# Kernel tuning notes

Measured on AMD Instinct MI355X. Metric: run time of the kernel, lower is better.

Reference implementation:

```python
import jax, jax.numpy as jnp
import numpy as np

N = 100000   # nodes
E = 1000000  # edges
G = 64       # graphs in batch
DIN, DH, DOUT = 128, 128, 64
BN_EPS = 1e-5


def setup_inputs() -> dict:
    key = jax.random.key(0)
    ks = jax.random.split(key, 20)
    inp = {}
    inp['x'] = jax.random.normal(ks[0], (N, DIN), dtype=jnp.float32)
    inp['edge_index'] = jax.random.randint(ks[1], (2, E), 0, N, dtype=jnp.int64)
    inp['batch'] = jnp.sort(jax.random.randint(ks[2], (N,), 0, G, dtype=jnp.int64))
    # GCN conv weights (stored [in, out]) + biases
    s = lambda k, i, o: jax.random.normal(k, (i, o), dtype=jnp.float32) / np.sqrt(i)
    inp['W1'] = s(ks[3], DIN, DH);  inp['b1'] = jnp.zeros((DH,), jnp.float32)
    inp['W2'] = s(ks[4], DH, DH);   inp['b2'] = jnp.zeros((DH,), jnp.float32)
    inp['W3'] = s(ks[5], DH, DOUT); inp['b3'] = jnp.zeros((DOUT,), jnp.float32)
    # BatchNorm params/buffers (eval mode)
    inp['g1'] = jnp.ones((DH,), jnp.float32);  inp['beta1'] = jnp.zeros((DH,), jnp.float32)
    inp['g2'] = jnp.ones((DH,), jnp.float32);  inp['beta2'] = jnp.zeros((DH,), jnp.float32)
    inp['mean1'] = jnp.zeros((DH,), jnp.float32); inp['var1'] = jnp.ones((DH,), jnp.float32)
    inp['mean2'] = jnp.zeros((DH,), jnp.float32); inp['var2'] = jnp.ones((DH,), jnp.float32)
    # GlobalAttention gate_nn: Linear(DOUT,DH) ReLU Linear(DH,1)
    inp['Wg1'] = s(ks[6], DOUT, DH); inp['bg1'] = jnp.zeros((DH,), jnp.float32)
    inp['Wg2'] = s(ks[7], DH, 1);    inp['bg2'] = jnp.zeros((1,), jnp.float32)
    # head MLP: Linear(DOUT,DH) ReLU Linear(DH,DOUT)
    inp['Wm1'] = s(ks[8], DOUT, DH); inp['bm1'] = jnp.zeros((DH,), jnp.float32)
    inp['Wm2'] = s(ks[9], DH, DOUT); inp['bm2'] = jnp.zeros((DOUT,), jnp.float32)
    return inp


def _gcn_conv(x, W, b, src, dst):
    # PyG GCNConv: add self-loops, sym-normalize, linear, scatter-sum, bias
    h = x @ W                                            # [N, out]
    deg = jnp.ones((N,), h.dtype).at[dst].add(1.0)       # in-degree + self-loop
    dinv = jax.lax.rsqrt(deg)
    norm = dinv[src] * dinv[dst]                         # [E]
    msg = h[src] * norm[:, None]                         # gather + scale
    out = jax.ops.segment_sum(msg, dst, num_segments=N)  # scatter
    out = out + h * (dinv * dinv)[:, None]               # self-loop term
    return out + b


def _bn(x, g, beta, mean, var):
    return (x - mean) * jax.lax.rsqrt(var + BN_EPS) * g + beta


def reference(x, edge_index, batch, W1, b1, W2, b2, W3, b3,
              g1, beta1, g2, beta2, mean1, var1, mean2, var2,
              Wg1, bg1, Wg2, bg2, Wm1, bm1, Wm2, bm2):
    src, dst = edge_index[0], edge_index[1]
    h = jax.nn.relu(_bn(_gcn_conv(x, W1, b1, src, dst), g1, beta1, mean1, var1))
    h = jax.nn.relu(_bn(_gcn_conv(h, W2, b2, src, dst), g2, beta2, mean2, var2))
    h = _gcn_conv(h, W3, b3, src, dst)                   # [N, DOUT]
    # GlobalAttention pooling: per-graph softmax of gate scores
    gate = jax.nn.relu(h @ Wg1 + bg1) @ Wg2 + bg2        # [N, 1]
    gate = gate[:, 0]
    m = jax.ops.segment_max(gate, batch, num_segments=G)
    e = jnp.exp(gate - m[batch])
    s = jax.ops.segment_sum(e, batch, num_segments=G)
    a = e / s[batch]                                     # [N]
    pooled = jax.ops.segment_sum(h * a[:, None], batch, num_segments=G)  # [G, DOUT]
    # MLP head (dropout off in eval)
    return jax.nn.relu(pooled @ Wm1 + bm1) @ Wm2 + bm2   # [G, DOUT]
```

## Files before the change

kernel.cpp:

```cpp
#include <hip/hip_runtime.h>
#include <hip/hip_bf16.h>
#include <hip/hip_fp16.h>
#include <math.h>

#define NN 100000
#define EE 1000000
#define GG 64
#define BN_EPS 1e-5f
#define CPB 16
#define EB 4096
#define NBLK ((EE + EB - 1) / EB)
#define NBUCK ((NN + 511) / 512)

typedef __attribute__((ext_vector_type(8))) short bf16x8;
typedef __attribute__((ext_vector_type(4))) float f32x4;

__device__ inline short f2bf(float f) {
  unsigned u = __float_as_uint(f);
  u = u + 0x7fff + ((u >> 16) & 1);
  return (short)(u >> 16);
}
__device__ inline float bf2f(short h) {
  return __uint_as_float(((unsigned)(unsigned short)h) << 16);
}

__device__ inline unsigned fenc(float f) {
  int b = __float_as_int(f);
  return (b < 0) ? ~(unsigned)b : ((unsigned)b | 0x80000000u);
}
__device__ inline float fdec(unsigned u) {
  int b = (u & 0x80000000u) ? (int)(u & 0x7fffffffu) : (int)~u;
  return __int_as_float(b);
}

__device__ inline void acc2(float& a0, float& a1, unsigned u) {
  asm("v_fma_mix_f32 %0, %2, 1.0, %0 op_sel:[0,0,0] op_sel_hi:[1,0,0]\n\t"
      "v_fma_mix_f32 %1, %2, 1.0, %1 op_sel:[1,0,0] op_sel_hi:[1,0,0]"
      : "+v"(a0), "+v"(a1)
      : "v"(u));
}
__device__ inline void acc8(float* a, uint4 u) {
  acc2(a[0], a[1], u.x);
  acc2(a[2], a[3], u.y);
  acc2(a[4], a[5], u.z);
  acc2(a[6], a[7], u.w);
}
__device__ inline uint4 zsel(uint4 u, int ok) {
  uint4 r;
  r.x = ok ? u.x : 0u;
  r.y = ok ? u.y : 0u;
  r.z = ok ? u.z : 0u;
  r.w = ok ? u.w : 0u;
  return r;
}

__global__ __launch_bounds__(256) void k_bhist(const int* __restrict__ dst,
                                               int* __restrict__ bhist, int E) {
  __shared__ int h[256];
  int t = threadIdx.x;
  h[t] = 0;
  __syncthreads();
  int base = blockIdx.x * EB;
#pragma unroll
  for (int j = 0; j < EB / 256; ++j) {
    int i = base + j * 256 + t;
    if (i < E) atomicAdd(&h[dst[i] >> 9], 1);
  }
  __syncthreads();
  bhist[blockIdx.x * 256 + t] = h[t];
}

__global__ __launch_bounds__(256) void k_bscan1(int* __restrict__ bhist,
                                                int* __restrict__ btot) {
  __shared__ int s[256];
  int bin = blockIdx.x, t = threadIdx.x;
  int v = (t < NBLK) ? bhist[t * 256 + bin] : 0;
  s[t] = v;
  __syncthreads();
  for (int o = 1; o < 256; o <<= 1) {
    int u = (t >= o) ? s[t - o] : 0;
    __syncthreads();
    s[t] += u;
    __syncthreads();
  }
  if (t < NBLK) bhist[t * 256 + bin] = s[t] - v;
  if (t == 255) btot[bin] = s[255];
}

__global__ __launch_bounds__(256) void k_bscan2(const int* __restrict__ btot,
                                                int* __restrict__ bstart) {
  __shared__ int s[256];
  int t = threadIdx.x;
  int v = btot[t];
  s[t] = v;
  __syncthreads();
  for (int o = 1; o < 256; o <<= 1) {
    int u = (t >= o) ? s[t - o] : 0;
    __syncthreads();
    s[t] += u;
    __syncthreads();
  }
  bstart[t] = s[t] - v;
}

__global__ __launch_bounds__(256) void k_bscat(const int* __restrict__ src,
                                               const int* __restrict__ dst,
                                               const int* __restrict__ bhist,
                                               const int* __restrict__ bstart,
                                               int2* __restrict__ pairs, int E) {
  __shared__ int h[256];
  __shared__ int base[256];
  int t = threadIdx.x;
  h[t] = 0;
  __syncthreads();
  int b0 = blockIdx.x * EB;
  int ds[EB / 256], rk[EB / 256];
#pragma unroll
  for (int j = 0; j < EB / 256; ++j) {
    int i = b0 + j * 256 + t;
    if (i < E) {
      int d = dst[i];
      ds[j] = d;
      rk[j] = atomicAdd(&h[d >> 9], 1);
    } else
      ds[j] = -1;
  }
  __syncthreads();
  base[t] = bstart[t] + bhist[blockIdx.x * 256 + t];
  __syncthreads();
#pragma unroll
  for (int j = 0; j < EB / 256; ++j) {
    int i = b0 + j * 256 + t;
    if (ds[j] >= 0) {
      int pos = base[ds[j] >> 9] + rk[j];
      pairs[pos] = make_int2(src[i], ds[j]);
    }
  }
}

__global__ __launch_bounds__(256) void k_bfill(const int2* __restrict__ pairs,
                                               const int* __restrict__ bstart,
                                               int* __restrict__ rowstart,
                                               int* __restrict__ eidx,
                                               float* __restrict__ dinv, int N,
                                               int E) {
  __shared__ int h[512];
  __shared__ int ex[512];
  __shared__ int ps[256];
  const int b = blockIdx.x;
  const int n0 = b << 9;
  const int e0 = bstart[b], e1 = bstart[b + 1];
  const int t = threadIdx.x;
  h[t] = 0;
  h[t + 256] = 0;
  __syncthreads();
  for (int i = e0 + t; i < e1; i += 256) atomicAdd(&h[pairs[i].y - n0], 1);
  __syncthreads();
  int v0 = h[2 * t], v1 = h[2 * t + 1];
  int sp = v0 + v1;
  ps[t] = sp;
  __syncthreads();
  for (int o = 1; o < 256; o <<= 1) {
    int u = (t >= o) ? ps[t - o] : 0;
    __syncthreads();
    ps[t] += u;
    __syncthreads();
  }
  int ex0 = ps[t] - sp;
  ex[2 * t] = ex0;
  ex[2 * t + 1] = ex0 + v0;
  __syncthreads();
  for (int i = t; i < 512; i += 256) {
    int node = n0 + i;
    if (node < N) {
      rowstart[node] = e0 + ex[i];
      dinv[node] = rsqrtf(1.0f + (float)h[i]);
    }
  }
  if (b == 0 && t == 0) rowstart[N] = E;
  __syncthreads();
  for (int i = e0 + t; i < e1; i += 256) {
    int2 p = pairs[i];
    int r = atomicAdd(&ex[p.y - n0], 1);
    eidx[e0 + r] = p.x;
  }
}

__global__ __launch_bounds__(256) void k_wsplit(const float* __restrict__ W1,
                                                const float* __restrict__ W2,
                                                const float* __restrict__ W3,
                                                const float* __restrict__ Wg1,
                                                short* __restrict__ wt) {
  int i = blockIdx.x * 256 + threadIdx.x;
  const float* W;
  short *hi, *lo;
  int K, M, idx;
  if (i < 16384) {
    W = W1; hi = wt; lo = wt + 16384; K = 128; M = 128; idx = i;
  } else if (i < 32768) {
    W = W2; hi = wt + 32768; lo = wt + 49152; K = 128; M = 128; idx = i - 16384;
  } else if (i < 40960) {
    W = W3; hi = wt + 65536; lo = wt + 73728; K = 128; M = 64; idx = i - 32768;
  } else {
    W = Wg1; hi = wt + 81920; lo = wt + 90112; K = 64; M = 128; idx = i - 40960;
  }
  int k = idx / M, n = idx % M;
  float w = W[idx];
  short h = f2bf(w);
  hi[n * K + k] = h;
  lo[n * K + k] = f2bf(w - bf2f(h));
}

__global__ __launch_bounds__(256) void k_bnprep(
    const float* __restrict__ g1, const float* __restrict__ b1,
    const float* __restrict__ m1, const float* __restrict__ v1,
    const float* __restrict__ g2, const float* __restrict__ b2,
    const float* __restrict__ m2, const float* __restrict__ v2,
    float* __restrict__ s1, float* __restrict__ h1, float* __restrict__ s2,
    float* __restrict__ h2) {
  int i = threadIdx.x;
  if (i < 128) {
    float s = g1[i] * rsqrtf(v1[i] + BN_EPS);
    s1[i] = s;
    h1[i] = b1[i] - m1[i] * s;
  } else {
    int j = i - 128;
    float s = g2[j] * rsqrtf(v2[j] + BN_EPS);
    s2[j] = s;
    h2[j] = b2[j] - m2[j] * s;
  }
}

template <int K, int M, int CTB, int AIN, int DINV, int GATE, int OUTH>
__device__ __forceinline__ void mgemm_body(
    short* lds, const float* __restrict__ Xf, const short* __restrict__ Xhi,
    const short* __restrict__ Xlo, const short* __restrict__ Wthi,
    const short* __restrict__ Wtlo, const float* __restrict__ dinv,
    const float* __restrict__ gbias, const float* __restrict__ Wg2v,
    const float* __restrict__ bg2v, void* __restrict__ Y,
    float* __restrict__ gate, int nrows) {
  constexpr int NC = K / 32;
  constexpr int KP = K + 8;
  constexpr int R = 2;
  const int lane = threadIdx.x & 63;
  const int wave = threadIdx.x >> 6;
  const int m16 = lane & 15;
  const int quad = lane >> 4;
  const int rowbase = blockIdx.x * 128 + wave * 32;
  const int cbase = blockIdx.y * CTB * 16;

  bf16x8 ahi[R][NC], alo[R][NC];
#pragma unroll
  for (int t = 0; t < R; ++t) {
    const int arow = rowbase + t * 16 + m16;
    const bool rok = arow < nrows;
#pragma unroll
    for (int c = 0; c < NC; ++c) {
      const int k0 = c * 32 + quad * 8;
      if constexpr (AIN) {
        if (rok) {
          ahi[t][c] = *(const bf16x8*)(Xhi + (size_t)arow * K + k0);
          alo[t][c] = *(const bf16x8*)(Xlo + (size_t)arow * K + k0);
        } else {
          ahi[t][c] = bf16x8{0, 0, 0, 0, 0, 0, 0, 0};
          alo[t][c] = bf16x8{0, 0, 0, 0, 0, 0, 0, 0};
        }
      } else {
        float4 v0 = make_float4(0.f, 0.f, 0.f, 0.f), v1 = v0;
        if (rok) {
          v0 = *(const float4*)(Xf + (size_t)arow * K + k0);
          v1 = *(const float4*)(Xf + (size_t)arow * K + k0 + 4);
        }
        float vv[8] = {v0.x, v0.y, v0.z, v0.w, v1.x, v1.y, v1.z, v1.w};
#pragma unroll
        for (int j = 0; j < 8; ++j) {
          short h = f2bf(vv[j]);
          ahi[t][c][j] = h;
          alo[t][c][j] = f2bf(vv[j] - bf2f(h));
        }
      }
    }
  }

  {
    constexpr int ELEMS = CTB * 16 * K;
#pragma unroll
    for (int i = threadIdx.x * 8; i < ELEMS; i += 256 * 8) {
      const int r = i / K, c = i % K;
      *(bf16x8*)(&lds[r * KP + c]) =
          *(const bf16x8*)(Wthi + (size_t)(cbase + r) * K + c);
      *(bf16x8*)(&lds[CTB * 16 * KP + r * KP + c]) =
          *(const bf16x8*)(Wtlo + (size_t)(cbase + r) * K + c);
    }
  }

  float dv[R][4];
  if constexpr (DINV && !GATE) {
#pragma unroll
    for (int t = 0; t < R; ++t)
#pragma unroll
      for (int r = 0; r < 4; ++r) {
        int row = rowbase + t * 16 + quad * 4 + r;
        dv[t][r] = (row < nrows) ? dinv[row] : 0.f;
      }
  }

  float gp[R][4];
  if constexpr (GATE) {
#pragma unroll
    for (int t = 0; t < R; ++t)
#pragma unroll
      for (int r = 0; r < 4; ++r) gp[t][r] = 0.f;
  }

  __syncthreads();

  f32x4 accs[CTB][R];
#pragma unroll
  for (int ct = 0; ct < CTB; ++ct) {
    bf16x8 bhi[NC], blo[NC];
    const int wrow = (ct * 16 + m16) * KP + quad * 8;
#pragma unroll
    for (int c = 0; c < NC; ++c) {
      bhi[c] = *(const bf16x8*)(&lds[wrow + c * 32]);
      blo[c] = *(const bf16x8*)(&lds[CTB * 16 * KP + wrow + c * 32]);
    }
#pragma unroll
    for (int t = 0; t < R; ++t) {
      f32x4 acc = {0.f, 0.f, 0.f, 0.f};
#pragma unroll
      for (int c = 0; c < NC; ++c) {
        acc = __builtin_amdgcn_mfma_f32_16x16x32_bf16(ahi[t][c], bhi[c], acc, 0, 0, 0);
        acc = __builtin_amdgcn_mfma_f32_16x16x32_bf16(ahi[t][c], blo[c], acc, 0, 0, 0);
        acc = __builtin_amdgcn_mfma_f32_16x16x32_bf16(alo[t][c], bhi[c], acc, 0, 0, 0);
      }
      if constexpr (GATE) {
        const int col = cbase + ct * 16 + m16;
        const float gb = gbias[col], wg = Wg2v[col];
#pragma unroll
        for (int r = 0; r < 4; ++r) gp[t][r] += fmaxf(acc[r] + gb, 0.f) * wg;
      } else {
        accs[ct][t] = acc;
      }
    }
  }

  if constexpr (GATE) {
#pragma unroll
    for (int o = 1; o < 16; o <<= 1) {
#pragma unroll
      for (int t = 0; t < R; ++t)
#pragma unroll
        for (int r = 0; r < 4; ++r) gp[t][r] += __shfl_xor(gp[t][r], o, 64);
    }
    if (m16 == 0) {
      const float b2 = bg2v[0];
#pragma unroll
      for (int t = 0; t < R; ++t)
#pragma unroll
        for (int r = 0; r < 4; ++r) {
          const int row = rowbase + t * 16 + quad * 4 + r;
          if (row < nrows) gate[row] = gp[t][r] + b2;
        }
    }
  } else {
    constexpr int COLS = CTB * 16;
    constexpr int SP = COLS + 8;
    __syncthreads();
#pragma unroll
    for (int ct = 0; ct < CTB; ++ct)
#pragma unroll
      for (int t = 0; t < R; ++t)
#pragma unroll
        for (int r = 0; r < 4; ++r) {
          const int row_l = wave * 32 + t * 16 + quad * 4 + r;
          float v = accs[ct][t][r];
          if constexpr (DINV) v *= dv[t][r];
          __half hv = __float2half(v);
          lds[row_l * SP + ct * 16 + m16] = *(short*)&hv;
        }
    __syncthreads();
    constexpr int TOT = 128 * COLS;
#pragma unroll
    for (int p = 0; p < TOT / (256 * 8); ++p) {
      const int idx8 = (p * 256 + threadIdx.x) * 8;
      const int row_l = idx8 / COLS;
      const int col0 = idx8 % COLS;
      const int grow = blockIdx.x * 128 + row_l;
      if (grow < nrows) {
        bf16x8 v = *(const bf16x8*)(&lds[row_l * SP + col0]);
        *(bf16x8*)((__half*)Y + (size_t)grow * M + cbase + col0) = v;
      }
    }
  }
}

#define MGEMM_ARGS                                                            \
  const float *Xf, const short *Xhi, const short *Xlo, const short *Wthi,     \
      const short *Wtlo, const float *dinv, const float *gbias,               \
      const float *Wg2v, const float *bg2v, void *Y, float *gate, int nrows

#define DEF_MGEMM(NAME, K, M, CTB, AIN, DINV, GATE, OUTH)                     \
  __global__ __launch_bounds__(256, 3) void NAME(MGEMM_ARGS) {                \
    __shared__ short lds[2 * CTB * 16 * (K + 8)];                             \
    mgemm_body<K, M, CTB, AIN, DINV, GATE, OUTH>(lds, Xf, Xhi, Xlo, Wthi,     \
                                                 Wtlo, dinv, gbias, Wg2v,     \
                                                 bg2v, Y, gate, nrows);       \
  }

DEF_MGEMM(k_mgemm1, 128, 128, 4, 0, 1, 0, 1)
DEF_MGEMM(k_mgemm2, 128, 128, 4, 1, 1, 0, 1)
DEF_MGEMM(k_mgemm3, 128, 64, 4, 1, 1, 0, 1)
DEF_MGEMM(k_mgemmg, 64, 128, 8, 0, 0, 1, 0)

template <int M, int EPI>
__device__ __forceinline__ void agg_body(
    const __half* __restrict__ hp, const int* __restrict__ rowstart,
    const int* __restrict__ eidx, const float* __restrict__ dinv,
    const float* __restrict__ bias, const float* __restrict__ bns,
    const float* __restrict__ bnh, float* __restrict__ outf,
    short* __restrict__ ohi, short* __restrict__ olo, int N) {
  constexpr int LPR = M / 8;
  constexpr int NPW = 64 / (2 * LPR);
  const int wv = (blockIdx.x * 256 + threadIdx.x) >> 6;
  const int lane = threadIdx.x & 63;
  const int grp = lane / (2 * LPR);
  const int slot = (lane / LPR) & 1;
  const int sub = lane % LPR;
  const int w = wv * NPW + grp;
  if (w >= N) return;
  const unsigned subo = (unsigned)sub * 16u;
  const float di = dinv[w];
  const int lo = rowstart[w], hi = rowstart[w + 1];
  const int hi1 = hi - 1;
  const char* hpb = (const char*)hp;
  float a[8] = {0.f, 0.f, 0.f, 0.f, 0.f, 0.f, 0.f, 0.f};

  int e = lo + slot;
  while (e < hi) {
    int idx[8], ss[8];
    uint4 uu[8];
#pragma unroll
    for (int p = 0; p < 8; ++p) {
      idx[p] = e + 2 * p;
      ss[p] = eidx[min(idx[p], hi1)];
    }
#pragma unroll
    for (int p = 0; p < 8; ++p)
      uu[p] = *(const uint4*)(hpb + ((unsigned)ss[p] * (unsigned)(M * 2) + subo));
#pragma unroll
    for (int p = 0; p < 8; ++p) {
      uu[p] = zsel(uu[p], idx[p] < hi);
      acc8(a, uu[p]);
    }
    e += 16;
  }
#pragma unroll
  for (int j = 0; j < 8; ++j) a[j] += __shfl_xor(a[j], LPR, 64);

  if (slot != 0) return;
  uint4 us = *(const uint4*)(hpb + ((unsigned)w * (unsigned)(M * 2) + subo));
  acc8(a, us);
  float4 b0 = *(const float4*)(bias + sub * 8);
  float4 b1 = *(const float4*)(bias + sub * 8 + 4);
  float r[8];
  r[0] = a[0] * di + b0.x;
  r[1] = a[1] * di + b0.y;
  r[2] = a[2] * di + b0.z;
  r[3] = a[3] * di + b0.w;
  r[4] = a[4] * di + b1.x;
  r[5] = a[5] * di + b1.y;
  r[6] = a[6] * di + b1.z;
  r[7] = a[7] * di + b1.w;
  if constexpr (EPI) {
    float4 s0 = *(const float4*)(bns + sub * 8);
    float4 s1 = *(const float4*)(bns + sub * 8 + 4);
    float4 h0 = *(const float4*)(bnh + sub * 8);
    float4 h1 = *(const float4*)(bnh + sub * 8 + 4);
    float sv[8] = {s0.x, s0.y, s0.z, s0.w, s1.x, s1.y, s1.z, s1.w};
    float hv[8] = {h0.x, h0.y, h0.z, h0.w, h1.x, h1.y, h1.z, h1.w};
    short hs[8], ls[8];
#pragma unroll
    for (int j = 0; j < 8; ++j) {
      float ev = fmaxf(r[j] * sv[j] + hv[j], 0.f);
      short hb = f2bf(ev);
      float res = ev - bf2f(hb);
      hs[j] = hb;
      ls[j] = (short)(__float_as_uint(res) >> 16);
    }
    *(short4*)(ohi + (size_t)w * M + sub * 8) = make_short4(hs[0], hs[1], hs[2], hs[3]);
    *(short4*)(ohi + (size_t)w * M + sub * 8 + 4) = make_short4(hs[4], hs[5], hs[6], hs[7]);
    *(short4*)(olo + (size_t)w * M + sub * 8) = make_short4(ls[0], ls[1], ls[2], ls[3]);
    *(short4*)(olo + (size_t)w * M + sub * 8 + 4) = make_short4(ls[4], ls[5], ls[6], ls[7]);
  } else {
    *(float4*)(outf + (size_t)w * M + sub * 8) = make_float4(r[0], r[1], r[2], r[3]);
    *(float4*)(outf + (size_t)w * M + sub * 8 + 4) = make_float4(r[4], r[5], r[6], r[7]);
  }
}

#define AGG_ARGS                                                              \
  const __half *hp, const int *rowstart, const int *eidx, const float *dinv,  \
      const float *bias, const float *bns, const float *bnh, float *outf,     \
      short *ohi, short *olo, int N

#define DEF_AGG(NAME, M, EPI)                                                 \
  __global__ __launch_bounds__(256) void NAME(AGG_ARGS) {                     \
    agg_body<M, EPI>(hp, rowstart, eidx, dinv, bias, bns, bnh, outf, ohi,     \
                     olo, N);                                                 \
  }

DEF_AGG(k_agg1, 128, 1)
DEF_AGG(k_agg2, 128, 1)
DEF_AGG(k_agg3, 64, 0)

__global__ __launch_bounds__(128) void k_gbounds(const int* __restrict__ batch,
                                                 int* __restrict__ gstart,
                                                 int N) {
  int g = threadIdx.x;
  if (g > GG) return;
  int lo = 0, hi = N;
  while (lo < hi) {
    int mid = (lo + hi) >> 1;
    if (batch[mid] < g) lo = mid + 1;
    else hi = mid;
  }
  gstart[g] = lo;
}

__global__ __launch_bounds__(256) void k_pmax(const float* __restrict__ gate,
                                              const int* __restrict__ gstart,
                                              unsigned* __restrict__ gmaxu) {
  __shared__ unsigned red[256];
  const int g = blockIdx.x / CPB;
  const int c = blockIdx.x % CPB;
  const int lo = gstart[g], hi = gstart[g + 1];
  const int len = hi - lo;
  const int b0 = lo + (int)(((long long)len * c) / CPB);
  const int b1 = lo + (int)(((long long)len * (c + 1)) / CPB);
  unsigned mx = 0u;
  for (int i = b0 + threadIdx.x; i < b1; i += 256) mx = max(mx, fenc(gate[i]));
  red[threadIdx.x] = mx;
  __syncthreads();
  for (int o = 128; o; o >>= 1) {
    if (threadIdx.x < o)
      red[threadIdx.x] = max(red[threadIdx.x], red[threadIdx.x + o]);
    __syncthreads();
  }
  if (threadIdx.x == 0 && red[0] != 0u) atomicMax(&gmaxu[g], red[0]);
}

__global__ __launch_bounds__(256) void k_psum(const float* __restrict__ gate,
                                              const float* __restrict__ h3,
                                              const unsigned* __restrict__ gmaxu,
                                              const int* __restrict__ gstart,
                                              float* __restrict__ pooledw,
                                              float* __restrict__ ssum) {
  __shared__ float accs[4][64];
  __shared__ float ses[4];
  const int g = blockIdx.x / CPB;
  const int c = blockIdx.x % CPB;
  const int lo = gstart[g], hi = gstart[g + 1];
  const int len = hi - lo;
  const int b0 = lo + (int)(((long long)len * c) / CPB);
  const int b1 = lo + (int)(((long long)len * (c + 1)) / CPB);
  const int wave = threadIdx.x >> 6, lane = threadIdx.x & 63;
  const float m = fdec(gmaxu[g]);
  float acc = 0.f, se = 0.f;
  for (int i = b0 + wave; i < b1; i += 4) {
    float e = expf(gate[i] - m);
    acc += e * h3[(size_t)i * 64 + lane];
    se += e;
  }
  accs[wave][lane] = acc;
  if (lane == 0) ses[wave] = se;
  __syncthreads();
  if (threadIdx.x < 64) {
    float a = accs[0][threadIdx.x] + accs[1][threadIdx.x] +
              accs[2][threadIdx.x] + accs[3][threadIdx.x];
    if (a != 0.f) atomicAdd(&pooledw[g * 64 + threadIdx.x], a);
  }
  if (threadIdx.x == 64) {
    float s = ses[0] + ses[1] + ses[2] + ses[3];
    if (s != 0.f) atomicAdd(&ssum[g], s);
  }
}

__global__ __launch_bounds__(256) void k_head(const float* __restrict__ pooledw,
                                              const float* __restrict__ ssum,
                                              const float* __restrict__ Wm1,
                                              const float* __restrict__ bm1,
                                              const float* __restrict__ Wm2,
                                              const float* __restrict__ bm2,
                                              float* __restrict__ out) {
  __shared__ float P[64 * 64];
  __shared__ float T[64 * 128];
  int tid = threadIdx.x;
  for (int i = tid; i < 4096; i += 256) {
    float s = ssum[i >> 6];
    P[i] = pooledw[i] * ((s > 0.f) ? 1.0f / s : 0.f);
  }
  __syncthreads();
  for (int e = tid; e < 8192; e += 256) {
    int r = e >> 7, c = e & 127;
    float a = bm1[c];
    for (int k = 0; k < 64; ++k) a += P[r * 64 + k] * Wm1[k * 128 + c];
    T[e] = fmaxf(a, 0.f);
  }
  __syncthreads();
  for (int e = tid; e < 4096; e += 256) {
    int r = e >> 6, c = e & 63;
    float a = bm2[c];
    for (int k = 0; k < 128; ++k) a += T[r * 128 + k] * Wm2[k * 64 + c];
    out[e] = a;
  }
}

extern "C" void kernel_launch(void* const* d_in, const int* in_sizes, int n_in,
                              void* d_out, int out_size, void* d_ws,
                              size_t ws_size, hipStream_t stream) {
  const int N = NN, E = EE;
  const float* x = (const float*)d_in[0];
  const int* ei = (const int*)d_in[1];
  const int* batch = (const int*)d_in[2];
  const float* W1 = (const float*)d_in[3];
  const float* b1 = (const float*)d_in[4];
  const float* W2 = (const float*)d_in[5];
  const float* b2 = (const float*)d_in[6];
  const float* W3 = (const float*)d_in[7];
  const float* b3 = (const float*)d_in[8];
  const float* g1 = (const float*)d_in[9];
  const float* beta1 = (const float*)d_in[10];
  const float* g2 = (const float*)d_in[11];
  const float* beta2 = (const float*)d_in[12];
  const float* mean1 = (const float*)d_in[13];
  const float* var1 = (const float*)d_in[14];
  const float* mean2 = (const float*)d_in[15];
  const float* var2 = (const float*)d_in[16];
  const float* Wg1 = (const float*)d_in[17];
  const float* bg1 = (const float*)d_in[18];
  const float* Wg2 = (const float*)d_in[19];
  const float* bg2 = (const float*)d_in[20];
  const float* Wm1 = (const float*)d_in[21];
  const float* bm1 = (const float*)d_in[22];
  const float* Wm2 = (const float*)d_in[23];
  const float* bm2 = (const float*)d_in[24];
  float* out = (float*)d_out;

  const int* src = ei;
  const int* dst = ei + E;

  char* wsb = (char*)d_ws;
  size_t off = 0;
  auto alloc = [&](size_t elems) -> void* {
    void* p = wsb + off;
    off += elems * 4;
    return p;
  };
  int* rowstart = (int*)alloc(N + 4);
  int* eidx = (int*)alloc(E);
  int2* pairs = (int2*)alloc((size_t)E * 2);
  int* bhist = (int*)alloc(NBLK * 256 + 256);
  int* btot = (int*)alloc(256);
  int* bstart = (int*)alloc(256);
  float* dinv = (float*)alloc(N);
  float* gate = (float*)alloc(N);
  __half* hbuf = (__half*)alloc((size_t)N * 64);
  short* ahi_p = (short*)alloc((size_t)N * 64);
  short* alo_p = (short*)alloc((size_t)N * 64);
  float* fbuf = (float*)alloc((size_t)N * 64);
  short* wt = (short*)alloc(49152);
  float* bn1s = (float*)alloc(128);
  float* bn1h = (float*)alloc(128);
  float* bn2s = (float*)alloc(128);
  float* bn2h = (float*)alloc(128);
  float* pooledw = (float*)alloc(GG * 64);
  float* ssum = (float*)alloc(GG);
  unsigned* gmaxu = (unsigned*)alloc(GG);
  int* gstart = (int*)alloc(GG + 4);
  (void)ws_size;
  (void)n_in;
  (void)in_sizes;
  (void)out_size;

  hipMemsetAsync(pooledw, 0, (GG * 64 + GG + GG) * sizeof(float), stream);
  k_bhist<<<NBLK, 256, 0, stream>>>(dst, bhist, E);
  k_bscan1<<<256, 256, 0, stream>>>(bhist, btot);
  k_bscan2<<<1, 256, 0, stream>>>(btot, bstart);
  k_bscat<<<NBLK, 256, 0, stream>>>(src, dst, bhist, bstart, pairs, E);
  k_bfill<<<NBUCK, 256, 0, stream>>>(pairs, bstart, rowstart, eidx, dinv, N, E);

  k_wsplit<<<192, 256, 0, stream>>>(W1, W2, W3, Wg1, wt);
  k_bnprep<<<1, 256, 0, stream>>>(g1, beta1, mean1, var1, g2, beta2, mean2,
                                  var2, bn1s, bn1h, bn2s, bn2h);
  k_gbounds<<<1, 128, 0, stream>>>(batch, gstart, N);

  const int gbb = (N + 127) / 128;
  const int ab128 = (N + 7) / 8;
  const int ab64 = (N + 15) / 16;

  k_mgemm1<<<dim3(gbb, 2), 256, 0, stream>>>(
      x, nullptr, nullptr, wt, wt + 16384, dinv, nullptr, nullptr, nullptr,
      hbuf, nullptr, N);
  k_agg1<<<ab128, 256, 0, stream>>>(hbuf, rowstart, eidx, dinv, b1, bn1s,
                                    bn1h, nullptr, ahi_p, alo_p, N);

  k_mgemm2<<<dim3(gbb, 2), 256, 0, stream>>>(
      nullptr, ahi_p, alo_p, wt + 32768, wt + 49152, dinv, nullptr, nullptr,
      nullptr, hbuf, nullptr, N);
  k_agg2<<<ab128, 256, 0, stream>>>(hbuf, rowstart, eidx, dinv, b2, bn2s,
                                    bn2h, nullptr, ahi_p, alo_p, N);

  k_mgemm3<<<dim3(gbb, 1), 256, 0, stream>>>(
      nullptr, ahi_p, alo_p, wt + 65536, wt + 73728, dinv, nullptr, nullptr,
      nullptr, hbuf, nullptr, N);
  k_agg3<<<ab64, 256, 0, stream>>>(hbuf, rowstart, eidx, dinv, b3, nullptr,
                                   nullptr, fbuf, nullptr, nullptr, N);

  k_mgemmg<<<dim3(gbb, 1), 256, 0, stream>>>(
      fbuf, nullptr, nullptr, wt + 81920, wt + 90112, nullptr, bg1, Wg2, bg2,
      nullptr, gate, N);

  k_pmax<<<GG * CPB, 256, 0, stream>>>(gate, gstart, gmaxu);
  k_psum<<<GG * CPB, 256, 0, stream>>>(gate, fbuf, gmaxu, gstart, pooledw,
                                       ssum);

  k_head<<<1, 256, 0, stream>>>(pooledw, ssum, Wm1, bm1, Wm2, bm2, out);
}
```

Before: 462.8 us.

## Slice GCN feature buffers by 16-column chunks and aggregate per slice

GEMM outputs and the aggregation inputs/outputs now use a column-sliced layout: for each 16-column slice, features of all nodes are stored contiguously (32 bytes per node). The aggregation kernel assigns one slice per block, so each gather touches a small contiguous 32-byte segment and the per-slice working set fits better in cache. The cost is re-reading CSR indices and dinv once per slice and doing more, smaller random gathers. Separately, the weight-split, BN-prep, graph-bounds and memset launches are merged into one prep kernel to cut launch overhead.

```diff
diff --git a/kernel.cpp b/kernel.cpp
--- a/kernel.cpp
+++ b/kernel.cpp
@@ -186,48 +186,59 @@
   }
 }
 
-__global__ __launch_bounds__(256) void k_wsplit(const float* __restrict__ W1,
-                                                const float* __restrict__ W2,
-                                                const float* __restrict__ W3,
-                                                const float* __restrict__ Wg1,
-                                                short* __restrict__ wt) {
-  int i = blockIdx.x * 256 + threadIdx.x;
-  const float* W;
-  short *hi, *lo;
-  int K, M, idx;
-  if (i < 16384) {
-    W = W1; hi = wt; lo = wt + 16384; K = 128; M = 128; idx = i;
-  } else if (i < 32768) {
-    W = W2; hi = wt + 32768; lo = wt + 49152; K = 128; M = 128; idx = i - 16384;
-  } else if (i < 40960) {
-    W = W3; hi = wt + 65536; lo = wt + 73728; K = 128; M = 64; idx = i - 32768;
+__global__ __launch_bounds__(256) void k_prep(
+    const float* __restrict__ W1, const float* __restrict__ W2,
+    const float* __restrict__ W3, const float* __restrict__ Wg1,
+    short* __restrict__ wt, const float* __restrict__ g1,
+    const float* __restrict__ b1, const float* __restrict__ m1,
+    const float* __restrict__ v1, const float* __restrict__ g2,
+    const float* __restrict__ b2, const float* __restrict__ m2,
+    const float* __restrict__ v2, float* __restrict__ s1,
+    float* __restrict__ h1, float* __restrict__ s2, float* __restrict__ h2,
+    const int* __restrict__ batch, int* __restrict__ gstart,
+    float* __restrict__ pooledw, int N) {
+  const int b = blockIdx.x, t = threadIdx.x;
+  if (b < 192) {
+    int i = b * 256 + t;
+    const float* W;
+    short *hi, *lo;
+    int K, M, idx;
+    if (i < 16384) {
+      W = W1; hi = wt; lo = wt + 16384; K = 128; M = 128; idx = i;
+    } else if (i < 32768) {
+      W = W2; hi = wt + 32768; lo = wt + 49152; K = 128; M = 128; idx = i - 16384;
+    } else if (i < 40960) {
+      W = W3; hi = wt + 65536; lo = wt + 73728; K = 128; M = 64; idx = i - 32768;
+    } else {
+      W = Wg1; hi = wt + 81920; lo = wt + 90112; K = 64; M = 128; idx = i - 40960;
+    }
+    int k = idx / M, n = idx % M;
+    float w = W[idx];
+    short h = f2bf(w);
+    hi[n * K + k] = h;
+    lo[n * K + k] = f2bf(w - bf2f(h));
+  } else if (b == 192) {
+    if (t < 128) {
+      float s = g1[t] * rsqrtf(v1[t] + BN_EPS);
+      s1[t] = s;
+      h1[t] = b1[t] - m1[t] * s;
+    } else {
+      int j = t - 128;
+      float s = g2[j] * rsqrtf(v2[j] + BN_EPS);
+      s2[j] = s;
+      h2[j] = b2[j] - m2[j] * s;
+    }
   } else {
-    W = Wg1; hi = wt + 81920; lo = wt + 90112; K = 64; M = 128; idx = i - 40960;
-  }
-  int k = idx / M, n = idx % M;
-  float w = W[idx];
-  short h = f2bf(w);
-  hi[n * K + k] = h;
-  lo[n * K + k] = f2bf(w - bf2f(h));
-}
-
-__global__ __launch_bounds__(256) void k_bnprep(
-    const float* __restrict__ g1, const float* __restrict__ b1,
-    const float* __restrict__ m1, const float* __restrict__ v1,
-    const float* __restrict__ g2, const float* __restrict__ b2,
-    const float* __restrict__ m2, const float* __restrict__ v2,
-    float* __restrict__ s1, float* __restrict__ h1, float* __restrict__ s2,
-    float* __restrict__ h2) {
-  int i = threadIdx.x;
-  if (i < 128) {
-    float s = g1[i] * rsqrtf(v1[i] + BN_EPS);
-    s1[i] = s;
-    h1[i] = b1[i] - m1[i] * s;
-  } else {
-    int j = i - 128;
-    float s = g2[j] * rsqrtf(v2[j] + BN_EPS);
-    s2[j] = s;
-    h2[j] = b2[j] - m2[j] * s;
+    if (t <= GG) {
+      int lo = 0, hi = N;
+      while (lo < hi) {
+        int mid = (lo + hi) >> 1;
+        if (batch[mid] < t) lo = mid + 1;
+        else hi = mid;
+      }
+      gstart[t] = lo;
+    }
+    for (int i = t; i < GG * 64 + GG + GG; i += 256) pooledw[i] = 0.f;
   }
 }
 
@@ -259,8 +270,9 @@
       const int k0 = c * 32 + quad * 8;
       if constexpr (AIN) {
         if (rok) {
-          ahi[t][c] = *(const bf16x8*)(Xhi + (size_t)arow * K + k0);
-          alo[t][c] = *(const bf16x8*)(Xlo + (size_t)arow * K + k0);
+          const size_t sa = ((size_t)(k0 >> 4) * nrows + arow) * 16 + (k0 & 8);
+          ahi[t][c] = *(const bf16x8*)(Xhi + sa);
+          alo[t][c] = *(const bf16x8*)(Xlo + sa);
         } else {
           ahi[t][c] = bf16x8{0, 0, 0, 0, 0, 0, 0, 0};
           alo[t][c] = bf16x8{0, 0, 0, 0, 0, 0, 0, 0};
@@ -389,7 +401,10 @@
       const int grow = blockIdx.x * 128 + row_l;
       if (grow < nrows) {
         bf16x8 v = *(const bf16x8*)(&lds[row_l * SP + col0]);
-        *(bf16x8*)((__half*)Y + (size_t)grow * M + cbase + col0) = v;
+        const size_t sa =
+            ((size_t)(blockIdx.y * (COLS >> 4) + (col0 >> 4)) * nrows + grow) *
+                16 + (col0 & 8);
+        *(bf16x8*)((__half*)Y + sa) = v;
       }
     }
   }
@@ -413,27 +428,26 @@
 DEF_MGEMM(k_mgemm3, 128, 64, 4, 1, 1, 0, 1)
 DEF_MGEMM(k_mgemmg, 64, 128, 8, 0, 0, 1, 0)
 
-template <int M, int EPI>
-__device__ __forceinline__ void agg_body(
+template <int NS, int EPI>
+__device__ __forceinline__ void aggs_body(
     const __half* __restrict__ hp, const int* __restrict__ rowstart,
     const int* __restrict__ eidx, const float* __restrict__ dinv,
     const float* __restrict__ bias, const float* __restrict__ bns,
     const float* __restrict__ bnh, float* __restrict__ outf,
     short* __restrict__ ohi, short* __restrict__ olo, int N) {
-  constexpr int LPR = M / 8;
-  constexpr int NPW = 64 / (2 * LPR);
-  const int wv = (blockIdx.x * 256 + threadIdx.x) >> 6;
+  const int slice = blockIdx.x % NS;
+  const int ng = blockIdx.x / NS;
   const int lane = threadIdx.x & 63;
-  const int grp = lane / (2 * LPR);
-  const int slot = (lane / LPR) & 1;
-  const int sub = lane % LPR;
-  const int w = wv * NPW + grp;
+  const int wv = threadIdx.x >> 6;
+  const int grp = lane >> 2;
+  const int slot = (lane >> 1) & 1;
+  const int sub = lane & 1;
+  const int w = ng * 64 + wv * 16 + grp;
   if (w >= N) return;
-  const unsigned subo = (unsigned)sub * 16u;
+  const char* hpb = (const char*)(hp + (size_t)slice * N * 16);
   const float di = dinv[w];
   const int lo = rowstart[w], hi = rowstart[w + 1];
   const int hi1 = hi - 1;
-  const char* hpb = (const char*)hp;
   float a[8] = {0.f, 0.f, 0.f, 0.f, 0.f, 0.f, 0.f, 0.f};
 
   int e = lo + slot;
@@ -447,7 +461,7 @@
     }
 #pragma unroll
     for (int p = 0; p < 8; ++p)
-      uu[p] = *(const uint4*)(hpb + ((unsigned)ss[p] * (unsigned)(M * 2) + subo));
+      uu[p] = *(const uint4*)(hpb + ((size_t)ss[p] * 32 + sub * 16));
 #pragma unroll
     for (int p = 0; p < 8; ++p) {
       uu[p] = zsel(uu[p], idx[p] < hi);
@@ -456,13 +470,14 @@
     e += 16;
   }
 #pragma unroll
-  for (int j = 0; j < 8; ++j) a[j] += __shfl_xor(a[j], LPR, 64);
+  for (int j = 0; j < 8; ++j) a[j] += __shfl_xor(a[j], 2, 64);
 
   if (slot != 0) return;
-  uint4 us = *(const uint4*)(hpb + ((unsigned)w * (unsigned)(M * 2) + subo));
+  uint4 us = *(const uint4*)(hpb + ((size_t)w * 32 + sub * 16));
   acc8(a, us);
-  float4 b0 = *(const float4*)(bias + sub * 8);
-  float4 b1 = *(const float4*)(bias + sub * 8 + 4);
+  const int fb = slice * 16 + sub * 8;
+  float4 b0 = *(const float4*)(bias + fb);
+  float4 b1 = *(const float4*)(bias + fb + 4);
   float r[8];
   r[0] = a[0] * di + b0.x;
   r[1] = a[1] * di + b0.y;
@@ -473,10 +488,10 @@
   r[6] = a[6] * di + b1.z;
   r[7] = a[7] * di + b1.w;
   if constexpr (EPI) {
-    float4 s0 = *(const float4*)(bns + sub * 8);
-    float4 s1 = *(const float4*)(bns + sub * 8 + 4);
-    float4 h0 = *(const float4*)(bnh + sub * 8);
-    float4 h1 = *(const float4*)(bnh + sub * 8 + 4);
+    float4 s0 = *(const float4*)(bns + fb);
+    float4 s1 = *(const float4*)(bns + fb + 4);
+    float4 h0 = *(const float4*)(bnh + fb);
+    float4 h1 = *(const float4*)(bnh + fb + 4);
     float sv[8] = {s0.x, s0.y, s0.z, s0.w, s1.x, s1.y, s1.z, s1.w};
     float hv[8] = {h0.x, h0.y, h0.z, h0.w, h1.x, h1.y, h1.z, h1.w};
     short hs[8], ls[8];
@@ -488,13 +503,15 @@
       hs[j] = hb;
       ls[j] = (short)(__float_as_uint(res) >> 16);
     }
-    *(short4*)(ohi + (size_t)w * M + sub * 8) = make_short4(hs[0], hs[1], hs[2], hs[3]);
-    *(short4*)(ohi + (size_t)w * M + sub * 8 + 4) = make_short4(hs[4], hs[5], hs[6], hs[7]);
-    *(short4*)(olo + (size_t)w * M + sub * 8) = make_short4(ls[0], ls[1], ls[2], ls[3]);
-    *(short4*)(olo + (size_t)w * M + sub * 8 + 4) = make_short4(ls[4], ls[5], ls[6], ls[7]);
+    const size_t oa = ((size_t)slice * N + w) * 16 + sub * 8;
+    *(short4*)(ohi + oa) = make_short4(hs[0], hs[1], hs[2], hs[3]);
+    *(short4*)(ohi + oa + 4) = make_short4(hs[4], hs[5], hs[6], hs[7]);
+    *(short4*)(olo + oa) = make_short4(ls[0], ls[1], ls[2], ls[3]);
+    *(short4*)(olo + oa + 4) = make_short4(ls[4], ls[5], ls[6], ls[7]);
   } else {
-    *(float4*)(outf + (size_t)w * M + sub * 8) = make_float4(r[0], r[1], r[2], r[3]);
-    *(float4*)(outf + (size_t)w * M + sub * 8 + 4) = make_float4(r[4], r[5], r[6], r[7]);
+    const size_t oa = (size_t)w * 64 + slice * 16 + sub * 8;
+    *(float4*)(outf + oa) = make_float4(r[0], r[1], r[2], r[3]);
+    *(float4*)(outf + oa + 4) = make_float4(r[4], r[5], r[6], r[7]);
   }
 }
 
@@ -503,29 +520,15 @@
       const float *bias, const float *bns, const float *bnh, float *outf,     \
       short *ohi, short *olo, int N
 
-#define DEF_AGG(NAME, M, EPI)                                                 \
+#define DEF_AGG(NAME, NS, EPI)                                                \
   __global__ __launch_bounds__(256) void NAME(AGG_ARGS) {                     \
-    agg_body<M, EPI>(hp, rowstart, eidx, dinv, bias, bns, bnh, outf, ohi,     \
-                     olo, N);                                                 \
-  }
-
-DEF_AGG(k_agg1, 128, 1)
-DEF_AGG(k_agg2, 128, 1)
-DEF_AGG(k_agg3, 64, 0)
-
-__global__ __launch_bounds__(128) void k_gbounds(const int* __restrict__ batch,
-                                                 int* __restrict__ gstart,
-                                                 int N) {
-  int g = threadIdx.x;
-  if (g > GG) return;
-  int lo = 0, hi = N;
-  while (lo < hi) {
-    int mid = (lo + hi) >> 1;
-    if (batch[mid] < g) lo = mid + 1;
-    else hi = mid;
-  }
-  gstart[g] = lo;
-}
+    aggs_body<NS, EPI>(hp, rowstart, eidx, dinv, bias, bns, bnh, outf, ohi,   \
+                       olo, N);                                               \
+  }
+
+DEF_AGG(k_agg1, 8, 1)
+DEF_AGG(k_agg2, 8, 1)
+DEF_AGG(k_agg3, 4, 0)
 
 __global__ __launch_bounds__(256) void k_pmax(const float* __restrict__ gate,
                                               const int* __restrict__ gstart,
@@ -682,39 +685,38 @@
   (void)in_sizes;
   (void)out_size;
 
-  hipMemsetAsync(pooledw, 0, (GG * 64 + GG + GG) * sizeof(float), stream);
   k_bhist<<<NBLK, 256, 0, stream>>>(dst, bhist, E);
   k_bscan1<<<256, 256, 0, stream>>>(bhist, btot);
   k_bscan2<<<1, 256, 0, stream>>>(btot, bstart);
   k_bscat<<<NBLK, 256, 0, stream>>>(src, dst, bhist, bstart, pairs, E);
   k_bfill<<<NBUCK, 256, 0, stream>>>(pairs, bstart, rowstart, eidx, dinv, N, E);
 
-  k_wsplit<<<192, 256, 0, stream>>>(W1, W2, W3, Wg1, wt);
-  k_bnprep<<<1, 256, 0, stream>>>(g1, beta1, mean1, var1, g2, beta2, mean2,
-                                  var2, bn1s, bn1h, bn2s, bn2h);
-  k_gbounds<<<1, 128, 0, stream>>>(batch, gstart, N);
+  k_prep<<<194, 256, 0, stream>>>(W1, W2, W3, Wg1, wt, g1, beta1, mean1, var1,
+                                  g2, beta2, mean2, var2, bn1s, bn1h, bn2s,
+                                  bn2h, batch, gstart, pooledw, N);
 
   const int gbb = (N + 127) / 128;
-  const int ab128 = (N + 7) / 8;
-  const int ab64 = (N + 15) / 16;
+  const int ngrp = (N + 63) / 64;
+  const int ab8 = 8 * ngrp;
+  const int ab4 = 4 * ngrp;
 
   k_mgemm1<<<dim3(gbb, 2), 256, 0, stream>>>(
       x, nullptr, nullptr, wt, wt + 16384, dinv, nullptr, nullptr, nullptr,
       hbuf, nullptr, N);
-  k_agg1<<<ab128, 256, 0, stream>>>(hbuf, rowstart, eidx, dinv, b1, bn1s,
-                                    bn1h, nullptr, ahi_p, alo_p, N);
+  k_agg1<<<ab8, 256, 0, stream>>>(hbuf, rowstart, eidx, dinv, b1, bn1s, bn1h,
+                                  nullptr, ahi_p, alo_p, N);
 
   k_mgemm2<<<dim3(gbb, 2), 256, 0, stream>>>(
       nullptr, ahi_p, alo_p, wt + 32768, wt + 49152, dinv, nullptr, nullptr,
       nullptr, hbuf, nullptr, N);
-  k_agg2<<<ab128, 256, 0, stream>>>(hbuf, rowstart, eidx, dinv, b2, bn2s,
-                                    bn2h, nullptr, ahi_p, alo_p, N);
+  k_agg2<<<ab8, 256, 0, stream>>>(hbuf, rowstart, eidx, dinv, b2, bn2s, bn2h,
+                                  nullptr, ahi_p, alo_p, N);
 
   k_mgemm3<<<dim3(gbb, 1), 256, 0, stream>>>(
       nullptr, ahi_p, alo_p, wt + 65536, wt + 73728, dinv, nullptr, nullptr,
       nullptr, hbuf, nullptr, N);
-  k_agg3<<<ab64, 256, 0, stream>>>(hbuf, rowstart, eidx, dinv, b3, nullptr,
-                                   nullptr, fbuf, nullptr, nullptr, N);
+  k_agg3<<<ab4, 256, 0, stream>>>(hbuf, rowstart, eidx, dinv, b3, nullptr,
+                                  nullptr, fbuf, nullptr, nullptr, N);
 
   k_mgemmg<<<dim3(gbb, 1), 256, 0, stream>>>(
       fbuf, nullptr, nullptr, wt + 81920, wt + 90112, nullptr, bg1, Wg2, bg2,
```

After: 468.1 us. No clear change (+1.2%).
